# Performance work log

Hardware: AMD Instinct MI355X
Metric: run time of the kernel (lower is better)

Reference implementation:

```python
import jax, jax.numpy as jnp
import numpy as np

EPS = 1e-7  # eps used inside bbox_iou
LAMBDA_BBOX = 1.0
LAMBDA_CLS = 1.0


def _coords(b):
    x, y, w, h = b[..., 0], b[..., 1], b[..., 2], b[..., 3]
    return x - w / 2, y - h / 2, x + w / 2, y + h / 2


def _pairwise_giou_loss(pred, target):
    # pred [B,T,4] -> [B,T,1,4]; target [B,O,4] -> [B,1,O,4]; broadcast to [B,T,O]
    b1x1, b1y1, b1x2, b1y2 = _coords(pred[:, :, None, :])
    b2x1, b2y1, b2x2, b2y2 = _coords(target[:, None, :, :])
    w1, h1 = b1x2 - b1x1, b1y2 - b1y1 + EPS
    w2, h2 = b2x2 - b2x1, b2y2 - b2y1 + EPS
    inter = jnp.clip(jnp.minimum(b1x2, b2x2) - jnp.maximum(b1x1, b2x1), 0) * \
            jnp.clip(jnp.minimum(b1y2, b2y2) - jnp.maximum(b1y1, b2y1), 0)
    union = w1 * h1 + w2 * h2 - inter + EPS
    iou = inter / union
    cw = jnp.maximum(b1x2, b2x2) - jnp.minimum(b1x1, b2x1)
    ch = jnp.maximum(b1y2, b2y2) - jnp.minimum(b1y1, b2y1)
    c_area = cw * ch + EPS
    giou = iou - (c_area - union) / c_area
    return 1.0 - giou  # [B,T,O]


def _lsa_rows(c):
    # Jonker-Volgenant shortest augmenting path (same algorithm as scipy's
    # linear_sum_assignment). c is [n, m] with n <= m; returns col4row [n].
    n, m = c.shape
    u = np.zeros(n)
    v = np.zeros(m)
    col4row = np.full(n, -1, np.int64)
    row4col = np.full(m, -1, np.int64)
    for cur in range(n):
        shortest = np.full(m, np.inf)
        path = np.full(m, -1, np.int64)
        SR = np.zeros(n, bool)
        SC = np.zeros(m, bool)
        min_val = 0.0
        i = cur
        sink = -1
        while sink == -1:
            SR[i] = True
            r = min_val + c[i] - u[i] - v
            upd = (~SC) & (r < shortest)
            shortest[upd] = r[upd]
            path[upd] = i
            masked = np.where(SC, np.inf, shortest)
            j = int(np.argmin(masked))
            min_val = masked[j]
            SC[j] = True
            if row4col[j] == -1:
                sink = j
            else:
                i = row4col[j]
        u[cur] += min_val
        sr = SR.copy(); sr[cur] = False
        u[sr] += min_val - shortest[col4row[sr]]
        v[SC] -= min_val - shortest[SC]
        j = sink
        while True:
            i = path[j]
            row4col[j] = i
            col4row[i], j = j, col4row[i]
            if i == cur:
                break
    return col4row


def _hungarian_np(cost):
    # Host callback; sequential per-batch like the original scipy loop.
    cost = np.asarray(cost, np.float64)
    B, T, O = cost.shape
    pred_idx = np.zeros((B, O), np.int32)
    tgt_idx = np.zeros((B, O), np.int32)
    for b in range(B):
        col4row = _lsa_rows(cost[b].T)  # assign each target (O rows) a token
        order = np.argsort(col4row)      # sort by pred index like scipy output
        pred_idx[b] = col4row[order].astype(np.int32)
        tgt_idx[b] = order.astype(np.int32)
    return pred_idx, tgt_idx


def _cost_matrix(pred_bboxes, target_bboxes, pred_classes, target_classes):
    B, T, C = pred_classes.shape
    O = target_classes.shape[1]
    log_probs = jax.nn.log_softmax(pred_classes, axis=-1)              # [B,T,C]
    idx = jnp.broadcast_to(target_classes[:, None, :], (B, T, O))      # [B,T,O]
    cls_neg_log = -jnp.take_along_axis(log_probs, idx, axis=-1)        # [B,T,O]
    ciou_loss = _pairwise_giou_loss(pred_bboxes, target_bboxes)        # [B,T,O]
    return LAMBDA_BBOX * ciou_loss + LAMBDA_CLS * cls_neg_log


def setup_inputs() -> dict:
    key = jax.random.key(0)
    k1, k2, k3, k4 = jax.random.split(key, 4)
    B, T, O, C = 32, 2048, 128, 80
    return {
        "pred_bboxes": jax.random.uniform(k1, (B, T, 4), dtype=jnp.float32),
        "target_bboxes": jax.random.uniform(k2, (B, O, 4), dtype=jnp.float32),
        "pred_classes": jax.random.normal(k3, (B, T, C), dtype=jnp.float32),
        "target_classes": jax.random.randint(k4, (B, O), 0, C, dtype=jnp.int32),
    }


def reference(pred_bboxes, target_bboxes, pred_classes, target_classes):
    cost = _cost_matrix(pred_bboxes, target_bboxes, pred_classes, target_classes)
    B, _, O = cost.shape
    out_spec = (jax.ShapeDtypeStruct((B, O), jnp.int32),
                jax.ShapeDtypeStruct((B, O), jnp.int32))
    pred_idx, tgt_idx = jax.pure_callback(_hungarian_np, out_spec, cost)
    return pred_idx, tgt_idx
```

## Files before the change

### kernel.cpp

```cpp
#include <hip/hip_runtime.h>
#include <math.h>
#include <float.h>

#define BB 32
#define TT 2048
#define OO 128
#define CC 80
#define EPSF 1e-7f
#define NT 256
#define SLOTS 8
#define CPAD 81
#define NTILE 8

struct alignas(16) URow { double u; int row; int pad; };
struct alignas(8)  P2   { int i; int j; };
struct alignas(16) Cand { double v; int j; int pad; };

template<int CTRL>
__device__ __forceinline__ void dpp_lexmin(double& bv, int& bj) {
    int lo = __double2loint(bv), hi = __double2hiint(bv);
    int tlo = __builtin_amdgcn_update_dpp(0, lo, CTRL, 0xF, 0xF, false);
    int thi = __builtin_amdgcn_update_dpp(0x7FF00000, hi, CTRL, 0xF, 0xF, false);
    int tj  = __builtin_amdgcn_update_dpp(0x7FFFFFFF, bj, CTRL, 0xF, 0xF, false);
    double tv = __hiloint2double(thi, tlo);
    if (tv <= bv) { bv = tv; bj = tj; }
}

template<int CTRL>
__device__ __forceinline__ void dpp_lexmin_f32(float& bv, int& bj) {
    int tlo = __builtin_amdgcn_update_dpp(0x7F800000, __float_as_int(bv), CTRL, 0xF, 0xF, false);
    int tj  = __builtin_amdgcn_update_dpp(0x7FFFFFFF, bj, CTRL, 0xF, 0xF, false);
    float tv = __int_as_float(tlo);
    if (tv < bv || (tv == bv && tj < bj)) { bv = tv; bj = tj; }
}

union SM {
    struct {
        float  xv[NT * CPAD];
        float4 box[OO];
        float2 wt[OO];
        unsigned long long rmin[OO * 4];
    } c;
    struct {
        URow   urow[TT];
        P2     path2[TT];
        int    row4col[TT];
        int    claim[TT];
        int    col4row[OO];
        double u[OO];
        int    amin[OO];
        int    flag[OO];
        int    freelist[OO];
        int    selj[OO + 8];
        double selm[OO + 8];
        int    selrow[OO + 8];
        Cand   cand[2][4];
        int    nfree;
    } l;
};

__global__ __launch_bounds__(NT) void hung_fused_kernel(
    const float* __restrict__ pb, const float* __restrict__ tb,
    const float* __restrict__ cls, const int* __restrict__ tcls,
    float* __restrict__ cost, unsigned long long* __restrict__ rowmins,
    int* __restrict__ cnt, int* __restrict__ out) {
#pragma clang fp contract(off)
    __shared__ SM sm;

    int bx = blockIdx.x;
    int b = bx & 31;
    int tile = bx >> 5;
    int t0 = tile * NT;
    int tid = threadIdx.x;
    int lane = tid & 63;
    int wave = tid >> 6;

    {
        const float* cbase = cls + ((size_t)b * TT + t0) * CC;
        #pragma unroll
        for (int k = 0; k < CC / 4; ++k) {
            int idx4 = (k * NT + tid) * 4;
            float4 vv = *(const float4*)(cbase + idx4);
            int r = idx4 / CC;
            int c = idx4 - r * CC;
            float* dst = &sm.c.xv[r * CPAD + c];
            dst[0] = vv.x; dst[1] = vv.y; dst[2] = vv.z; dst[3] = vv.w;
        }
        if (tid < OO) {
            float4 tbox = ((const float4*)tb)[b * OO + tid];
            float x1 = tbox.x - tbox.z / 2.f;
            float y1 = tbox.y - tbox.w / 2.f;
            float x2 = tbox.x + tbox.z / 2.f;
            float y2 = tbox.y + tbox.w / 2.f;
            float4 bb; bb.x = x1; bb.y = y1; bb.z = x2; bb.w = y2;
            sm.c.box[tid] = bb;
            float w2 = x2 - x1;
            float h2 = (y2 - y1) + EPSF;
            float2 wt; wt.x = w2 * h2;
            wt.y = __int_as_float(tcls[b * OO + tid]);
            sm.c.wt[tid] = wt;
        }
        __syncthreads();

        size_t bt = (size_t)b * TT + t0 + tid;
        float4 pbox = ((const float4*)pb)[bt];
        float b1x1 = pbox.x - pbox.z / 2.f;
        float b1y1 = pbox.y - pbox.w / 2.f;
        float b1x2 = pbox.x + pbox.z / 2.f;
        float b1y2 = pbox.y + pbox.w / 2.f;
        float w1 = b1x2 - b1x1;
        float h1 = (b1y2 - b1y1) + EPSF;
        float w1h1 = w1 * h1;

        const float* xr = &sm.c.xv[tid * CPAD];
        float m = xr[0];
        #pragma unroll
        for (int c = 1; c < CC; ++c) m = fmaxf(m, xr[c]);
        float ssum = 0.f;
        #pragma unroll
        for (int c = 0; c < CC; ++c) ssum += expf(xr[c] - m);
        float ls = logf(ssum);

        float* cbt = cost + (size_t)b * OO * TT + t0;
        for (int o = 0; o < OO; ++o) {
            float4 bb = sm.c.box[o];
            float2 wt = sm.c.wt[o];
            float b2x1 = bb.x, b2y1 = bb.y, b2x2 = bb.z, b2y2 = bb.w;
            float iw = fminf(b1x2, b2x2) - fmaxf(b1x1, b2x1);
            float ih = fminf(b1y2, b2y2) - fmaxf(b1y1, b2y1);
            iw = fmaxf(iw, 0.f);
            ih = fmaxf(ih, 0.f);
            float inter = iw * ih;
            float uni = ((w1h1 + wt.x) - inter) + EPSF;
            float iou = inter / uni;
            float cw = fmaxf(b1x2, b2x2) - fminf(b1x1, b2x1);
            float ch = fmaxf(b1y2, b2y2) - fminf(b1y1, b2y1);
            float c_area = (cw * ch) + EPSF;
            float giou = iou - (c_area - uni) / c_area;
            float bbox_loss = 1.0f - giou;

            float xc = xr[__float_as_int(wt.y)];
            float shifted = xc - m;
            float cls_neg = -(shifted - ls);

            float cval = bbox_loss + cls_neg;
            cbt[(size_t)o * TT + tid] = cval;

            float bvv = cval;
            int bjj = t0 + tid;
            dpp_lexmin_f32<0x111>(bvv, bjj);
            dpp_lexmin_f32<0x112>(bvv, bjj);
            dpp_lexmin_f32<0x114>(bvv, bjj);
            dpp_lexmin_f32<0x118>(bvv, bjj);
            dpp_lexmin_f32<0x142>(bvv, bjj);
            dpp_lexmin_f32<0x143>(bvv, bjj);
            if (lane == 63)
                sm.c.rmin[o * 4 + wave] =
                    ((unsigned long long)__float_as_uint(bvv) << 32) | (unsigned)bjj;
        }
        __syncthreads();
        if (tid < OO) {
            unsigned long long r0 = sm.c.rmin[tid * 4 + 0];
            unsigned long long r1 = sm.c.rmin[tid * 4 + 1];
            unsigned long long r2 = sm.c.rmin[tid * 4 + 2];
            unsigned long long r3 = sm.c.rmin[tid * 4 + 3];
            unsigned long long m01 = r0 < r1 ? r0 : r1;
            unsigned long long m23 = r2 < r3 ? r2 : r3;
            rowmins[((size_t)b * NTILE + tile) * OO + tid] = m01 < m23 ? m01 : m23;
        }
        __syncthreads();
        if (tid == 0)
            __hip_atomic_fetch_add(&cnt[b], 1, __ATOMIC_RELEASE,
                                   __HIP_MEMORY_SCOPE_AGENT);
    }

    if (tile != 0) return;

    if (tid == 0) {
        while (__hip_atomic_load(&cnt[b], __ATOMIC_ACQUIRE,
                                 __HIP_MEMORY_SCOPE_AGENT) < NTILE)
            __builtin_amdgcn_s_sleep(2);
    }
    __syncthreads();

    const float* cb = cost + (size_t)b * OO * TT;
    const int jbase = tid * SLOTS;

    double v_[SLOTS];
    double key[SLOTS];
    #pragma unroll
    for (int s = 0; s < SLOTS; ++s) v_[s] = 0.0;

    if (tid < OO) {
        const unsigned long long* p = rowmins + (size_t)b * NTILE * OO + tid;
        unsigned long long best = p[0];
        #pragma unroll
        for (int t = 1; t < NTILE; ++t) {
            unsigned long long x = p[t * OO];
            if (x < best) best = x;
        }
        sm.l.u[tid] = (double)__uint_as_float((unsigned)(best >> 32));
        sm.l.amin[tid] = (int)(best & 0xFFFFFFFFull);
        sm.l.col4row[tid] = -1;
    }
    for (int j = tid; j < TT; j += NT) { sm.l.row4col[j] = -1; sm.l.claim[j] = 0x7FFFFFFF; }
    __syncthreads();

    if (tid < OO) atomicMin(&sm.l.claim[sm.l.amin[tid]], tid);
    __syncthreads();
    if (tid < OO) {
        int j = sm.l.amin[tid];
        if (sm.l.claim[j] == tid) { sm.l.col4row[tid] = j; sm.l.row4col[j] = tid; }
    }
    __syncthreads();

    for (int j = tid; j < TT; j += NT) {
        int r = sm.l.row4col[j];
        URow t; t.row = r; t.u = (r >= 0) ? sm.l.u[r] : 0.0; t.pad = 0;
        sm.l.urow[j] = t;
    }
    if (tid < OO) sm.l.flag[tid] = (sm.l.col4row[tid] < 0) ? 1 : 0;
    __syncthreads();
    if (tid < OO && sm.l.flag[tid]) {
        int rank = 0;
        for (int o = 0; o < tid; ++o) rank += sm.l.flag[o];
        sm.l.freelist[rank] = tid;
    }
    if (tid == 0) {
        int nf = 0;
        for (int o = 0; o < OO; ++o) nf += sm.l.flag[o];
        sm.l.nfree = nf;
    }
    __syncthreads();
    int nfree = sm.l.nfree;

    int par = 0;
    for (int fi = 0; fi < nfree; ++fi) {
        int cur = sm.l.freelist[fi];

        #pragma unroll
        for (int s = 0; s < SLOTS; ++s) key[s] = INFINITY;
        int selbits = 0;
        double mv = 0.0;
        int i = cur, jc = -1;
        double ui = sm.l.u[cur];
        const float* crow0 = cb + (size_t)i * TT + jbase;
        float4 c0 = *(const float4*)crow0;
        float4 c1 = *(const float4*)(crow0 + 4);
        int L = 0, sink;

        while (true) {
            float cv[SLOTS] = {c0.x, c0.y, c0.z, c0.w, c1.x, c1.y, c1.z, c1.w};

            double bv = INFINITY;
            int bj = TT;
            #pragma unroll
            for (int s = 0; s < SLOTS; ++s) {
                if (!((selbits >> s) & 1)) {
                    double r = ((mv + (double)cv[s]) - ui) - v_[s];
                    if (r < key[s]) {
                        key[s] = r;
                        P2 p; p.i = i; p.j = jc;
                        sm.l.path2[s * NT + tid] = p;
                    }
                    double kk = key[s];
                    if (kk < bv) { bv = kk; bj = jbase + s; }
                }
            }
            dpp_lexmin<0x111>(bv, bj);
            dpp_lexmin<0x112>(bv, bj);
            dpp_lexmin<0x114>(bv, bj);
            dpp_lexmin<0x118>(bv, bj);
            dpp_lexmin<0x142>(bv, bj);
            dpp_lexmin<0x143>(bv, bj);
            int rlo = __builtin_amdgcn_readlane(__double2loint(bv), 63);
            int rhi = __builtin_amdgcn_readlane(__double2hiint(bv), 63);
            double wv = __hiloint2double(rhi, rlo);
            int wj = __builtin_amdgcn_readlane(bj, 63);

            par ^= 1;
            if (lane == 0) {
                Cand c; c.v = wv; c.j = wj; c.pad = 0;
                sm.l.cand[par][wave] = c;
            }
            __syncthreads();

            Cand cc = sm.l.cand[par][0];
            double MV = cc.v; int BJ = cc.j;
            #pragma unroll
            for (int w = 1; w < 4; ++w) {
                Cand c2 = sm.l.cand[par][w];
                if (c2.v < MV || (c2.v == MV && c2.j < BJ)) { MV = c2.v; BJ = c2.j; }
            }
            mv = MV;
            if ((BJ >> 3) == tid) selbits |= 1 << (BJ & 7);
            if (tid == 0) sm.l.selj[L] = BJ;

            URow ur = sm.l.urow[BJ];
            if (ur.row < 0) { sink = BJ; break; }
            if (tid == 0) { sm.l.selm[L] = MV; sm.l.selrow[L] = ur.row; }
            i = ur.row; ui = ur.u; jc = BJ;
            L++;
            const float* crow = cb + (size_t)i * TT + jbase;
            c0 = *(const float4*)crow;
            c1 = *(const float4*)(crow + 4);
        }

        double M = mv;
        #pragma unroll
        for (int s = 0; s < SLOTS; ++s)
            if ((selbits >> s) & 1) v_[s] = v_[s] - (M - key[s]);
        for (int k = tid; k < L; k += NT)
            sm.l.u[sm.l.selrow[k]] = sm.l.u[sm.l.selrow[k]] + (M - sm.l.selm[k]);
        if (tid == 0) {
            sm.l.u[cur] = sm.l.u[cur] + M;
            int j = sink;
            while (true) {
                P2 p = sm.l.path2[(j & 7) * NT + (j >> 3)];
                int ii = p.i;
                sm.l.row4col[j] = ii;
                sm.l.col4row[ii] = j;
                if (ii == cur) break;
                j = p.j;
            }
        }
        __syncthreads();
        if (tid <= L) {
            int j = sm.l.selj[tid];
            int r = sm.l.row4col[j];
            URow t; t.u = sm.l.u[r]; t.row = r; t.pad = 0;
            sm.l.urow[j] = t;
        }
        __syncthreads();
    }

    if (tid < OO) {
        int my = sm.l.col4row[tid];
        int rank = 0;
        for (int o = 0; o < OO; ++o) rank += (sm.l.col4row[o] < my) ? 1 : 0;
        out[(size_t)b * OO + rank] = my;
        out[(size_t)(BB + b) * OO + rank] = tid;
    }
}

extern "C" void kernel_launch(void* const* d_in, const int* in_sizes, int n_in,
                              void* d_out, int out_size, void* d_ws, size_t ws_size,
                              hipStream_t stream) {
    const float* pred_bboxes = (const float*)d_in[0];
    const float* target_bboxes = (const float*)d_in[1];
    const float* pred_classes = (const float*)d_in[2];
    const int* target_classes = (const int*)d_in[3];
    int* out = (int*)d_out;

    float* cost = (float*)d_ws;
    unsigned long long* rowmins =
        (unsigned long long*)(cost + (size_t)BB * OO * TT);
    int* cnt = (int*)(rowmins + (size_t)BB * NTILE * OO);

    hipMemsetAsync(cnt, 0, BB * sizeof(int), stream);

    hung_fused_kernel<<<BB * NTILE, NT, 0, stream>>>(
        pred_bboxes, target_bboxes, pred_classes, target_classes,
        cost, rowmins, cnt, out);
}
```

Measured before the change: 289.5 us.

## Halve token tile, split objects across half-blocks, prefetch next free row

The cost-matrix phase now uses 128-token tiles with 16 tiles per batch, and the two halves of each block split the 128 objects between them. This doubles the grid and halves shared memory per block for more parallelism. Class logits are read with nontemporal loads. In the Hungarian phase the next free row's costs are prefetched before the augmenting-path loop, the reduced-cost expression is simplified by hoisting ui-mv, and urow lookups for all four wave candidates are issued before the argmin reduction to shorten the serial latency chain. The trade-off is that each token's softmax is computed twice (once per half-block), and the hoisted subtraction can change rounding slightly.

```diff
diff --git a/kernel.cpp b/kernel.cpp
--- a/kernel.cpp
+++ b/kernel.cpp
@@ -10,7 +10,10 @@
 #define NT 256
 #define SLOTS 8
 #define CPAD 81
-#define NTILE 8
+#define TPT 128
+#define NTILE 16
+
+typedef float vf4 __attribute__((ext_vector_type(4)));
 
 struct alignas(16) URow { double u; int row; int pad; };
 struct alignas(8)  P2   { int i; int j; };
@@ -36,10 +39,10 @@
 
 union SM {
     struct {
-        float  xv[NT * CPAD];
+        float  xv[TPT * CPAD];
         float4 box[OO];
         float2 wt[OO];
-        unsigned long long rmin[OO * 4];
+        unsigned long long rmin[OO * 2];
     } c;
     struct {
         URow   urow[TT];
@@ -70,17 +73,19 @@
     int bx = blockIdx.x;
     int b = bx & 31;
     int tile = bx >> 5;
-    int t0 = tile * NT;
+    int t0 = tile * TPT;
     int tid = threadIdx.x;
     int lane = tid & 63;
     int wave = tid >> 6;
+    int tok = tid & (TPT - 1);
+    int oh = tid >> 7;
 
     {
         const float* cbase = cls + ((size_t)b * TT + t0) * CC;
         #pragma unroll
-        for (int k = 0; k < CC / 4; ++k) {
+        for (int k = 0; k < (TPT * CC) / (NT * 4); ++k) {
             int idx4 = (k * NT + tid) * 4;
-            float4 vv = *(const float4*)(cbase + idx4);
+            vf4 vv = __builtin_nontemporal_load((const vf4*)(cbase + idx4));
             int r = idx4 / CC;
             int c = idx4 - r * CC;
             float* dst = &sm.c.xv[r * CPAD + c];
@@ -102,7 +107,7 @@
         }
         __syncthreads();
 
-        size_t bt = (size_t)b * TT + t0 + tid;
+        size_t bt = (size_t)b * TT + t0 + tok;
         float4 pbox = ((const float4*)pb)[bt];
         float b1x1 = pbox.x - pbox.z / 2.f;
         float b1y1 = pbox.y - pbox.w / 2.f;
@@ -112,7 +117,7 @@
         float h1 = (b1y2 - b1y1) + EPSF;
         float w1h1 = w1 * h1;
 
-        const float* xr = &sm.c.xv[tid * CPAD];
+        const float* xr = &sm.c.xv[tok * CPAD];
         float m = xr[0];
         #pragma unroll
         for (int c = 1; c < CC; ++c) m = fmaxf(m, xr[c]);
@@ -122,7 +127,8 @@
         float ls = logf(ssum);
 
         float* cbt = cost + (size_t)b * OO * TT + t0;
-        for (int o = 0; o < OO; ++o) {
+        for (int k = 0; k < OO / 2; ++k) {
+            int o = oh * (OO / 2) + k;
             float4 bb = sm.c.box[o];
             float2 wt = sm.c.wt[o];
             float b2x1 = bb.x, b2y1 = bb.y, b2x2 = bb.z, b2y2 = bb.w;
@@ -144,10 +150,10 @@
             float cls_neg = -(shifted - ls);
 
             float cval = bbox_loss + cls_neg;
-            cbt[(size_t)o * TT + tid] = cval;
+            cbt[(size_t)o * TT + tok] = cval;
 
             float bvv = cval;
-            int bjj = t0 + tid;
+            int bjj = t0 + tok;
             dpp_lexmin_f32<0x111>(bvv, bjj);
             dpp_lexmin_f32<0x112>(bvv, bjj);
             dpp_lexmin_f32<0x114>(bvv, bjj);
@@ -155,18 +161,14 @@
             dpp_lexmin_f32<0x142>(bvv, bjj);
             dpp_lexmin_f32<0x143>(bvv, bjj);
             if (lane == 63)
-                sm.c.rmin[o * 4 + wave] =
+                sm.c.rmin[o * 2 + (wave & 1)] =
                     ((unsigned long long)__float_as_uint(bvv) << 32) | (unsigned)bjj;
         }
         __syncthreads();
         if (tid < OO) {
-            unsigned long long r0 = sm.c.rmin[tid * 4 + 0];
-            unsigned long long r1 = sm.c.rmin[tid * 4 + 1];
-            unsigned long long r2 = sm.c.rmin[tid * 4 + 2];
-            unsigned long long r3 = sm.c.rmin[tid * 4 + 3];
-            unsigned long long m01 = r0 < r1 ? r0 : r1;
-            unsigned long long m23 = r2 < r3 ? r2 : r3;
-            rowmins[((size_t)b * NTILE + tile) * OO + tid] = m01 < m23 ? m01 : m23;
+            unsigned long long r0 = sm.c.rmin[tid * 2 + 0];
+            unsigned long long r1 = sm.c.rmin[tid * 2 + 1];
+            rowmins[((size_t)b * NTILE + tile) * OO + tid] = r0 < r1 ? r0 : r1;
         }
         __syncthreads();
         if (tid == 0)
@@ -233,6 +235,13 @@
     }
     __syncthreads();
     int nfree = sm.l.nfree;
+
+    float4 pf0, pf1;
+    if (nfree > 0) {
+        const float* rr = cb + (size_t)sm.l.freelist[0] * TT + jbase;
+        pf0 = *(const float4*)rr;
+        pf1 = *(const float4*)(rr + 4);
+    }
 
     int par = 0;
     for (int fi = 0; fi < nfree; ++fi) {
@@ -244,20 +253,19 @@
         double mv = 0.0;
         int i = cur, jc = -1;
         double ui = sm.l.u[cur];
-        const float* crow0 = cb + (size_t)i * TT + jbase;
-        float4 c0 = *(const float4*)crow0;
-        float4 c1 = *(const float4*)(crow0 + 4);
+        float4 c0 = pf0, c1 = pf1;
         int L = 0, sink;
 
         while (true) {
             float cv[SLOTS] = {c0.x, c0.y, c0.z, c0.w, c1.x, c1.y, c1.z, c1.w};
+            double D = ui - mv;
 
             double bv = INFINITY;
             int bj = TT;
             #pragma unroll
             for (int s = 0; s < SLOTS; ++s) {
                 if (!((selbits >> s) & 1)) {
-                    double r = ((mv + (double)cv[s]) - ui) - v_[s];
+                    double r = ((double)cv[s] - D) - v_[s];
                     if (r < key[s]) {
                         key[s] = r;
                         P2 p; p.i = i; p.j = jc;
@@ -285,25 +293,35 @@
             }
             __syncthreads();
 
-            Cand cc = sm.l.cand[par][0];
-            double MV = cc.v; int BJ = cc.j;
-            #pragma unroll
-            for (int w = 1; w < 4; ++w) {
-                Cand c2 = sm.l.cand[par][w];
-                if (c2.v < MV || (c2.v == MV && c2.j < BJ)) { MV = c2.v; BJ = c2.j; }
-            }
+            Cand cc0 = sm.l.cand[par][0];
+            Cand cc1 = sm.l.cand[par][1];
+            Cand cc2 = sm.l.cand[par][2];
+            Cand cc3 = sm.l.cand[par][3];
+            URow u0 = sm.l.urow[cc0.j];
+            URow u1 = sm.l.urow[cc1.j];
+            URow u2 = sm.l.urow[cc2.j];
+            URow u3 = sm.l.urow[cc3.j];
+            double MV = cc0.v; int BJ = cc0.j; URow UW = u0;
+            if (cc1.v < MV || (cc1.v == MV && cc1.j < BJ)) { MV = cc1.v; BJ = cc1.j; UW = u1; }
+            if (cc2.v < MV || (cc2.v == MV && cc2.j < BJ)) { MV = cc2.v; BJ = cc2.j; UW = u2; }
+            if (cc3.v < MV || (cc3.v == MV && cc3.j < BJ)) { MV = cc3.v; BJ = cc3.j; UW = u3; }
             mv = MV;
             if ((BJ >> 3) == tid) selbits |= 1 << (BJ & 7);
             if (tid == 0) sm.l.selj[L] = BJ;
 
-            URow ur = sm.l.urow[BJ];
-            if (ur.row < 0) { sink = BJ; break; }
-            if (tid == 0) { sm.l.selm[L] = MV; sm.l.selrow[L] = ur.row; }
-            i = ur.row; ui = ur.u; jc = BJ;
+            if (UW.row < 0) { sink = BJ; break; }
+            if (tid == 0) { sm.l.selm[L] = MV; sm.l.selrow[L] = UW.row; }
+            i = UW.row; ui = UW.u; jc = BJ;
             L++;
             const float* crow = cb + (size_t)i * TT + jbase;
             c0 = *(const float4*)crow;
             c1 = *(const float4*)(crow + 4);
+        }
+
+        if (fi + 1 < nfree) {
+            const float* rr = cb + (size_t)sm.l.freelist[fi + 1] * TT + jbase;
+            pf0 = *(const float4*)rr;
+            pf1 = *(const float4*)(rr + 4);
         }
 
         double M = mv;
@@ -357,7 +375,7 @@
         (unsigned long long*)(cost + (size_t)BB * OO * TT);
     int* cnt = (int*)(rowmins + (size_t)BB * NTILE * OO);
 
-    hipMemsetAsync(cnt, 0, BB * sizeof(int), stream);
+    (void)hipMemsetAsync(cnt, 0, BB * sizeof(int), stream);
 
     hung_fused_kernel<<<BB * NTILE, NT, 0, stream>>>(
         pred_bboxes, target_bboxes, pred_classes, target_classes,
```

Measured after the change: 260.1 us. -10.1%, faster.
